# Kernel optimization log

Measured on AMD Instinct MI355X. Metric: run time of the kernel, lower is better.

Reference implementation:

```python
import jax, jax.numpy as jnp
import numpy as np


def setup_inputs() -> dict:
    key = jax.random.key(0)
    k1, k2, k3 = jax.random.split(key, 3)
    b, c, h, w = 4, 64, 64, 64
    content = jax.random.normal(k1, (b, c, h, w), dtype=jnp.float32)
    content_s = jax.random.normal(k2, (b, c, h, w), dtype=jnp.float32)
    style = jax.random.normal(k3, (b, c, h, w), dtype=jnp.float32)
    return {"content": content, "content_s": content_s, "style": style}


def reference(content, content_s, style):
    b, c, h, w = content.shape
    hw = h * w
    Fc = content.reshape(b, c, hw)      # [b, c, HW]
    Fs = content_s.reshape(b, c, hw)    # [b, c, HW]
    Fst = style.reshape(b, c, hw)       # [b, c, HW]
    # S[b, q, k] = sum_c Fc[b, c, q] * Fs[b, c, k]  (Fc transposed as in torch)
    S = jnp.einsum('bcq,bck->bqk', Fc, Fs)
    S = jax.nn.softmax(S, axis=-1)
    # O = style @ S^T : O[b, c, q] = sum_k Fst[b, c, k] * S[b, q, k]
    O = jnp.einsum('bck,bqk->bcq', Fst, S).reshape(b, c, h, w)
    return jnp.concatenate((content, O), axis=1)
```

## Files before the change

### kernel.cpp

```cpp
#include <hip/hip_runtime.h>
#include <math.h>


#define Bb 4
#define Cc 64
#define HWs 4096
#define RLOG2E 1.44269504088896340736f
#define DEFER_THR 6.0f

typedef _Float16 half8 __attribute__((ext_vector_type(8)));
typedef _Float16 half4 __attribute__((ext_vector_type(4)));
typedef float floatx4 __attribute__((ext_vector_type(4)));
typedef unsigned uint2v __attribute__((ext_vector_type(2)));

__global__ __launch_bounds__(256) void prep_k(const float* __restrict__ content,
                                              const float* __restrict__ Fs,
                                              const float* __restrict__ Fst,
                                              float* __restrict__ out,
                                              _Float16* __restrict__ Kt,
                                              _Float16* __restrict__ Vt) {
    const int bid = blockIdx.x;
    const int t = threadIdx.x;
    if (bid < 1024) {
        int i4 = bid * 256 + t;
        const float4* c4 = (const float4*)content;
        const float4* v4 = (const float4*)Fst;
        float4* o4 = (float4*)out;
        int b = i4 >> 16, rem = i4 & 65535;
        o4[(size_t)b * 131072 + rem] = c4[i4];
        float4 v = v4[i4];
        half4 h;
        h[0] = (_Float16)v.x; h[1] = (_Float16)v.y;
        h[2] = (_Float16)v.z; h[3] = (_Float16)v.w;
        *(half4*)(Vt + (size_t)i4 * 4) = h;
    } else {
        __shared__ _Float16 T[16][72];
        int e = bid - 1024;
        int b = e >> 8;
        int hw0 = (e & 255) * 16;
        const float* sb = Fs + (size_t)b * Cc * HWs;
        {
            int c = t >> 2, x4 = (t & 3) * 4;
            float4 v = *(const float4*)(sb + (size_t)c * HWs + hw0 + x4);
            T[x4 + 0][c] = (_Float16)v.x;
            T[x4 + 1][c] = (_Float16)v.y;
            T[x4 + 2][c] = (_Float16)v.z;
            T[x4 + 3][c] = (_Float16)v.w;
        }
        __syncthreads();
        if (t < 128) {
            int row = t >> 3, g = t & 7;
            _Float16* db = Kt + (size_t)b * HWs * Cc;
            *(half8*)(db + (size_t)(hw0 + row) * Cc + g * 8) = *(half8*)&T[row][g * 8];
        }
    }
}

template <int NS>
__global__ __launch_bounds__(256, 3) void attn_k(const float* __restrict__ Fc,
                                                 const _Float16* __restrict__ Kt,
                                                 const _Float16* __restrict__ Vt,
                                                 _Float16* __restrict__ Opart,
                                                 float2* __restrict__ ml) {
    constexpr int TPS = 64 / NS;
    const int tid  = threadIdx.x;
    const int w    = tid >> 6;
    const int lane = tid & 63;
    const int quad = lane >> 4;
    const int l15  = lane & 15;
    const int qg = blockIdx.x & 31;
    const int b  = (blockIdx.x >> 5) & 3;
    const int s  = blockIdx.x >> 7;
    const int k0base = s * TPS * 64;
    const int qA = qg * 128 + w * 32 + l15;
    const int qB = qA + 16;

    __shared__ _Float16 Kl[3][64 * 64];
    __shared__ _Float16 Vl[3][64 * 64];

    const float*    Fcb = Fc + (size_t)b * Cc * HWs;
    const _Float16* Kb  = Kt + (size_t)b * HWs * Cc;
    const _Float16* Vb  = Vt + (size_t)b * Cc * HWs;

    const int lrow = lane >> 3;
    const int lj   = lane & 7;
    const int lsw8 = (lj ^ lrow) * 8;
    const int r0   = w * 16;

    auto stage = [&](int kt, int p) {
        const int kk0 = k0base + kt * 64;
        #pragma unroll
        for (int c = 0; c < 2; ++c) {
            const int r = r0 + c * 8 + lrow;
            __builtin_amdgcn_global_load_lds(
                (const __attribute__((address_space(1))) void*)(Kb + (size_t)(kk0 + r) * 64 + lsw8),
                (__attribute__((address_space(3))) void*)&Kl[p][(r0 + c * 8) * 64],
                16, 0, 0);
            __builtin_amdgcn_global_load_lds(
                (const __attribute__((address_space(1))) void*)(Vb + (size_t)r * HWs + kk0 + lsw8),
                (__attribute__((address_space(3))) void*)&Vl[p][(r0 + c * 8) * 64],
                16, 0, 0);
        }
    };

    half8 qf[2][2];
    #pragma unroll
    for (int j = 0; j < 8; ++j) {
        qf[0][0][j] = (_Float16)(Fcb[(size_t)(quad * 8 + j) * HWs + qA] * RLOG2E);
        qf[0][1][j] = (_Float16)(Fcb[(size_t)(32 + quad * 8 + j) * HWs + qA] * RLOG2E);
        qf[1][0][j] = (_Float16)(Fcb[(size_t)(quad * 8 + j) * HWs + qB] * RLOG2E);
        qf[1][1][j] = (_Float16)(Fcb[(size_t)(32 + quad * 8 + j) * HWs + qB] * RLOG2E);
    }

    floatx4 acc[2][4];
    #pragma unroll
    for (int g = 0; g < 2; ++g)
        #pragma unroll
        for (int m = 0; m < 4; ++m) acc[g][m] = (floatx4)(0.0f);
    float m_run[2] = {-INFINITY, -INFINITY};
    float lsum[2] = {0.0f, 0.0f};

    asm volatile("" ::: "memory");
    stage(0, 0);
    stage(1, 1);

    const int swl = (l15 & 7);
    #pragma unroll
    for (int kt = 0; kt < TPS; ++kt) {
        const int p = kt % 3;
        if (kt + 1 < TPS) asm volatile("s_waitcnt vmcnt(4)" ::: "memory");
        else              asm volatile("s_waitcnt vmcnt(0)" ::: "memory");
        __builtin_amdgcn_s_barrier();
        __builtin_amdgcn_sched_barrier(0);
        if (kt + 2 < TPS) stage(kt + 2, (kt + 2) % 3);

        floatx4 sv[2][4];
        __builtin_amdgcn_s_setprio(1);
        #pragma unroll
        for (int m = 0; m < 4; ++m) {
            const half8 ka0 = *(const half8*)&Kl[p][(m * 16 + l15) * 64 + ((quad ^ swl) * 8)];
            const half8 ka1 = *(const half8*)&Kl[p][(m * 16 + l15) * 64 + (((4 + quad) ^ swl) * 8)];
            sv[0][m] = __builtin_amdgcn_mfma_f32_16x16x32_f16(ka0, qf[0][0], (floatx4)(0.0f), 0, 0, 0);
            sv[0][m] = __builtin_amdgcn_mfma_f32_16x16x32_f16(ka1, qf[0][1], sv[0][m], 0, 0, 0);
            sv[1][m] = __builtin_amdgcn_mfma_f32_16x16x32_f16(ka0, qf[1][0], (floatx4)(0.0f), 0, 0, 0);
            sv[1][m] = __builtin_amdgcn_mfma_f32_16x16x32_f16(ka1, qf[1][1], sv[1][m], 0, 0, 0);
        }
        __builtin_amdgcn_s_setprio(0);

        half8 pb[2][2];
        #pragma unroll
        for (int g = 0; g < 2; ++g) {
            float mm[4];
            #pragma unroll
            for (int m = 0; m < 4; ++m)
                mm[m] = fmaxf(fmaxf(sv[g][m][0], sv[g][m][1]),
                              fmaxf(sv[g][m][2], sv[g][m][3]));
            float mx = fmaxf(fmaxf(mm[0], mm[1]), fmaxf(mm[2], mm[3]));
            {
                unsigned mu = __float_as_uint(mx);
                uint2v t32 = __builtin_amdgcn_permlane32_swap(mu, mu, false, false);
                mx = fmaxf(__uint_as_float(t32[0]), __uint_as_float(t32[1]));
                mu = __float_as_uint(mx);
                uint2v t16 = __builtin_amdgcn_permlane16_swap(mu, mu, false, false);
                mx = fmaxf(__uint_as_float(t16[0]), __uint_as_float(t16[1]));
            }
            if (!__all(mx - m_run[g] <= DEFER_THR)) {
                float m_new = fmaxf(m_run[g], mx);
                float alpha = exp2f(m_run[g] - m_new);
                m_run[g] = m_new;
                #pragma unroll
                for (int m = 0; m < 4; ++m) acc[g][m] *= alpha;
                lsum[g] *= alpha;
            }
            const float mb = m_run[g];
            unsigned Ap[4], Bp[4];
            #pragma unroll
            for (int m = 0; m < 4; ++m) {
                float e0 = exp2f(sv[g][m][0] - mb);
                float e1 = exp2f(sv[g][m][1] - mb);
                float e2 = exp2f(sv[g][m][2] - mb);
                float e3 = exp2f(sv[g][m][3] - mb);
                lsum[g] += (e0 + e1) + (e2 + e3);
                Ap[m] = __builtin_bit_cast(unsigned, __builtin_amdgcn_cvt_pkrtz(e0, e1));
                Bp[m] = __builtin_bit_cast(unsigned, __builtin_amdgcn_cvt_pkrtz(e2, e3));
            }
            unsigned pw[2][4];
            { uint2v a = __builtin_amdgcn_permlane32_swap(Ap[0], Ap[1], false, false);
              uint2v u = __builtin_amdgcn_permlane16_swap(a[0], a[1], false, false);
              pw[0][0] = u[0]; pw[0][2] = u[1]; }
            { uint2v a = __builtin_amdgcn_permlane32_swap(Bp[0], Bp[1], false, false);
              uint2v u = __builtin_amdgcn_permlane16_swap(a[0], a[1], false, false);
              pw[0][1] = u[0]; pw[0][3] = u[1]; }
            { uint2v a = __builtin_amdgcn_permlane32_swap(Ap[2], Ap[3], false, false);
              uint2v u = __builtin_amdgcn_permlane16_swap(a[0], a[1], false, false);
              pw[1][0] = u[0]; pw[1][2] = u[1]; }
            { uint2v a = __builtin_amdgcn_permlane32_swap(Bp[2], Bp[3], false, false);
              uint2v u = __builtin_amdgcn_permlane16_swap(a[0], a[1], false, false);
              pw[1][1] = u[0]; pw[1][3] = u[1]; }
            #pragma unroll
            for (int ks = 0; ks < 2; ++ks) {
                union { unsigned u4[4]; half8 h; } z;
                z.u4[0] = pw[ks][0]; z.u4[1] = pw[ks][1];
                z.u4[2] = pw[ks][2]; z.u4[3] = pw[ks][3];
                pb[g][ks] = z.h;
            }
        }

        __builtin_amdgcn_s_setprio(1);
        #pragma unroll
        for (int m = 0; m < 4; ++m) {
            const half8 va0 = *(const half8*)&Vl[p][(m * 16 + l15) * 64 + ((quad ^ swl) * 8)];
            const half8 va1 = *(const half8*)&Vl[p][(m * 16 + l15) * 64 + (((4 + quad) ^ swl) * 8)];
            acc[0][m] = __builtin_amdgcn_mfma_f32_16x16x32_f16(va0, pb[0][0], acc[0][m], 0, 0, 0);
            acc[0][m] = __builtin_amdgcn_mfma_f32_16x16x32_f16(va1, pb[0][1], acc[0][m], 0, 0, 0);
            acc[1][m] = __builtin_amdgcn_mfma_f32_16x16x32_f16(va0, pb[1][0], acc[1][m], 0, 0, 0);
            acc[1][m] = __builtin_amdgcn_mfma_f32_16x16x32_f16(va1, pb[1][1], acc[1][m], 0, 0, 0);
        }
        __builtin_amdgcn_s_setprio(0);
    }

    _Float16* op = Opart + ((size_t)(s * Bb + b) * Cc) * HWs;
    #pragma unroll
    for (int g = 0; g < 2; ++g) {
        lsum[g] += __shfl_xor(lsum[g], 16);
        lsum[g] += __shfl_xor(lsum[g], 32);
        int q = (g == 0) ? qA : qB;
        #pragma unroll
        for (int m = 0; m < 4; ++m)
            #pragma unroll
            for (int r = 0; r < 4; ++r) {
                int c = m * 16 + quad * 4 + r;
                op[(size_t)c * HWs + q] = (_Float16)acc[g][m][r];
            }
        if (quad == 0)
            ml[((size_t)b * HWs + q) * NS + s] = make_float2(m_run[g], lsum[g]);
    }
}

template <int NS>
__global__ __launch_bounds__(256) void combine_k(const _Float16* __restrict__ Opart,
                                                 const float2* __restrict__ ml,
                                                 float* __restrict__ out) {
    int idx = blockIdx.x * 256 + threadIdx.x;
    int q = idx & 4095;
    int c = (idx >> 12) & 63;
    int b = idx >> 18;
    const float2* mlp = ml + ((size_t)b * HWs + q) * NS;
    float2 mls[NS];
    #pragma unroll
    for (int s = 0; s < NS; ++s) mls[s] = mlp[s];
    float M = -INFINITY;
    #pragma unroll
    for (int s = 0; s < NS; ++s) M = fmaxf(M, mls[s].x);
    float l = 0.0f, o = 0.0f;
    #pragma unroll
    for (int s = 0; s < NS; ++s) {
        float wgt = exp2f(mls[s].x - M);
        l += wgt * mls[s].y;
        o += wgt * (float)Opart[(((size_t)s * Bb + b) * Cc + c) * HWs + q];
    }
    out[((size_t)b * 2 * Cc + Cc + c) * HWs + q] = o / l;
}

extern "C" void kernel_launch(void* const* d_in, const int* in_sizes, int n_in,
                              void* d_out, int out_size, void* d_ws, size_t ws_size,
                              hipStream_t stream) {
    const float* content   = (const float*)d_in[0];
    const float* content_s = (const float*)d_in[1];
    const float* style     = (const float*)d_in[2];
    float* out = (float*)d_out;

    _Float16* Kt = (_Float16*)d_ws;
    _Float16* Vt = Kt + (size_t)Bb * HWs * Cc;
    _Float16* Opart = Vt + (size_t)Bb * Cc * HWs;

    const size_t base = (size_t)2 * Bb * HWs * Cc * sizeof(_Float16);
    const size_t need8 = base + (size_t)8 * Bb * Cc * HWs * sizeof(_Float16)
                              + (size_t)Bb * HWs * 8 * sizeof(float2);
    const int ns = (ws_size >= need8) ? 8 : 4;
    float2* ml = (float2*)(Opart + (size_t)ns * Bb * Cc * HWs);

    prep_k<<<dim3(2048), dim3(256), 0, stream>>>(content, content_s, style, out, Kt, Vt);
    if (ns == 8) {
        attn_k<8><<<dim3(8 * Bb * 32), dim3(256), 0, stream>>>(content, Kt, Vt, Opart, ml);
        combine_k<8><<<dim3(4096), dim3(256), 0, stream>>>(Opart, ml, out);
    } else {
        attn_k<4><<<dim3(4 * Bb * 32), dim3(256), 0, stream>>>(content, Kt, Vt, Opart, ml);
        combine_k<4><<<dim3(4096), dim3(256), 0, stream>>>(Opart, ml, out);
    }
}
```

Before: 113.4 us.

## Software-pipeline QK MFMA one tile ahead and split K/V staging

Splits K and V staging so that K is prefetched three tiles ahead and V two tiles ahead, and computes the QK^T MFMAs for tile kt+1 before running softmax and PV for tile kt, using double-buffered score registers. The aim is to overlap matrix-core work with the exp/permlane softmax chain and hide load latency. It also moves the cross-lane max reduction inside the rescale branch, so the common path skips permlane swaps. In exchange it raises register pressure from a second score buffer, and the loop unrolled by two assumes TPS is even.

```diff
diff --git a/kernel.cpp b/kernel.cpp
--- a/kernel.cpp
+++ b/kernel.cpp
@@ -12,6 +12,9 @@
 typedef _Float16 half4 __attribute__((ext_vector_type(4)));
 typedef float floatx4 __attribute__((ext_vector_type(4)));
 typedef unsigned uint2v __attribute__((ext_vector_type(2)));
+
+#define GAS __attribute__((address_space(1)))
+#define LAS __attribute__((address_space(3)))
 
 __global__ __launch_bounds__(256) void prep_k(const float* __restrict__ content,
                                               const float* __restrict__ Fs,
@@ -87,19 +90,24 @@
     const int lsw8 = (lj ^ lrow) * 8;
     const int r0   = w * 16;
 
-    auto stage = [&](int kt, int p) {
+    auto stageK = [&](int kt) {
         const int kk0 = k0base + kt * 64;
         #pragma unroll
         for (int c = 0; c < 2; ++c) {
             const int r = r0 + c * 8 + lrow;
             __builtin_amdgcn_global_load_lds(
-                (const __attribute__((address_space(1))) void*)(Kb + (size_t)(kk0 + r) * 64 + lsw8),
-                (__attribute__((address_space(3))) void*)&Kl[p][(r0 + c * 8) * 64],
-                16, 0, 0);
+                (const GAS void*)(Kb + (size_t)(kk0 + r) * 64 + lsw8),
+                (LAS void*)&Kl[kt % 3][(r0 + c * 8) * 64], 16, 0, 0);
+        }
+    };
+    auto stageV = [&](int kt) {
+        const int kk0 = k0base + kt * 64;
+        #pragma unroll
+        for (int c = 0; c < 2; ++c) {
+            const int r = r0 + c * 8 + lrow;
             __builtin_amdgcn_global_load_lds(
-                (const __attribute__((address_space(1))) void*)(Vb + (size_t)r * HWs + kk0 + lsw8),
-                (__attribute__((address_space(3))) void*)&Vl[p][(r0 + c * 8) * 64],
-                16, 0, 0);
+                (const GAS void*)(Vb + (size_t)r * HWs + kk0 + lsw8),
+                (LAS void*)&Vl[kt % 3][(r0 + c * 8) * 64], 16, 0, 0);
         }
     };
 
@@ -120,52 +128,42 @@
     float m_run[2] = {-INFINITY, -INFINITY};
     float lsum[2] = {0.0f, 0.0f};
 
-    asm volatile("" ::: "memory");
-    stage(0, 0);
-    stage(1, 1);
-
-    const int swl = (l15 & 7);
-    #pragma unroll
-    for (int kt = 0; kt < TPS; ++kt) {
-        const int p = kt % 3;
-        if (kt + 1 < TPS) asm volatile("s_waitcnt vmcnt(4)" ::: "memory");
-        else              asm volatile("s_waitcnt vmcnt(0)" ::: "memory");
-        __builtin_amdgcn_s_barrier();
-        __builtin_amdgcn_sched_barrier(0);
-        if (kt + 2 < TPS) stage(kt + 2, (kt + 2) % 3);
-
-        floatx4 sv[2][4];
+    const int swl = l15 & 7;
+    const int o0 = (quad ^ swl) * 8;
+    const int o1 = ((4 + quad) ^ swl) * 8;
+
+    auto s_mfma = [&](int kt1, floatx4 (&sv)[2][4]) {
+        const _Float16* K = &Kl[kt1 % 3][0];
         __builtin_amdgcn_s_setprio(1);
         #pragma unroll
         for (int m = 0; m < 4; ++m) {
-            const half8 ka0 = *(const half8*)&Kl[p][(m * 16 + l15) * 64 + ((quad ^ swl) * 8)];
-            const half8 ka1 = *(const half8*)&Kl[p][(m * 16 + l15) * 64 + (((4 + quad) ^ swl) * 8)];
+            const half8 ka0 = *(const half8*)(K + (m * 16 + l15) * 64 + o0);
+            const half8 ka1 = *(const half8*)(K + (m * 16 + l15) * 64 + o1);
             sv[0][m] = __builtin_amdgcn_mfma_f32_16x16x32_f16(ka0, qf[0][0], (floatx4)(0.0f), 0, 0, 0);
             sv[0][m] = __builtin_amdgcn_mfma_f32_16x16x32_f16(ka1, qf[0][1], sv[0][m], 0, 0, 0);
             sv[1][m] = __builtin_amdgcn_mfma_f32_16x16x32_f16(ka0, qf[1][0], (floatx4)(0.0f), 0, 0, 0);
             sv[1][m] = __builtin_amdgcn_mfma_f32_16x16x32_f16(ka1, qf[1][1], sv[1][m], 0, 0, 0);
         }
         __builtin_amdgcn_s_setprio(0);
-
+    };
+
+    auto sm_pv = [&](int kt, floatx4 (&sv)[2][4]) {
         half8 pb[2][2];
         #pragma unroll
         for (int g = 0; g < 2; ++g) {
-            float mm[4];
-            #pragma unroll
-            for (int m = 0; m < 4; ++m)
-                mm[m] = fmaxf(fmaxf(sv[g][m][0], sv[g][m][1]),
-                              fmaxf(sv[g][m][2], sv[g][m][3]));
-            float mx = fmaxf(fmaxf(mm[0], mm[1]), fmaxf(mm[2], mm[3]));
-            {
+            float mm0 = fmaxf(fmaxf(sv[g][0][0], sv[g][0][1]), fmaxf(sv[g][0][2], sv[g][0][3]));
+            float mm1 = fmaxf(fmaxf(sv[g][1][0], sv[g][1][1]), fmaxf(sv[g][1][2], sv[g][1][3]));
+            float mm2 = fmaxf(fmaxf(sv[g][2][0], sv[g][2][1]), fmaxf(sv[g][2][2], sv[g][2][3]));
+            float mm3 = fmaxf(fmaxf(sv[g][3][0], sv[g][3][1]), fmaxf(sv[g][3][2], sv[g][3][3]));
+            float mx = fmaxf(fmaxf(mm0, mm1), fmaxf(mm2, mm3));
+            if (!__all(mx - m_run[g] <= DEFER_THR)) {
                 unsigned mu = __float_as_uint(mx);
                 uint2v t32 = __builtin_amdgcn_permlane32_swap(mu, mu, false, false);
-                mx = fmaxf(__uint_as_float(t32[0]), __uint_as_float(t32[1]));
-                mu = __float_as_uint(mx);
+                float wmx = fmaxf(__uint_as_float(t32[0]), __uint_as_float(t32[1]));
+                mu = __float_as_uint(wmx);
                 uint2v t16 = __builtin_amdgcn_permlane16_swap(mu, mu, false, false);
-                mx = fmaxf(__uint_as_float(t16[0]), __uint_as_float(t16[1]));
-            }
-            if (!__all(mx - m_run[g] <= DEFER_THR)) {
-                float m_new = fmaxf(m_run[g], mx);
+                wmx = fmaxf(__uint_as_float(t16[0]), __uint_as_float(t16[1]));
+                float m_new = fmaxf(m_run[g], wmx);
                 float alpha = exp2f(m_run[g] - m_new);
                 m_run[g] = m_new;
                 #pragma unroll
@@ -205,18 +203,45 @@
                 pb[g][ks] = z.h;
             }
         }
-
+        const _Float16* V = &Vl[kt % 3][0];
         __builtin_amdgcn_s_setprio(1);
         #pragma unroll
         for (int m = 0; m < 4; ++m) {
-            const half8 va0 = *(const half8*)&Vl[p][(m * 16 + l15) * 64 + ((quad ^ swl) * 8)];
-            const half8 va1 = *(const half8*)&Vl[p][(m * 16 + l15) * 64 + (((4 + quad) ^ swl) * 8)];
+            const half8 va0 = *(const half8*)(V + (m * 16 + l15) * 64 + o0);
+            const half8 va1 = *(const half8*)(V + (m * 16 + l15) * 64 + o1);
             acc[0][m] = __builtin_amdgcn_mfma_f32_16x16x32_f16(va0, pb[0][0], acc[0][m], 0, 0, 0);
             acc[0][m] = __builtin_amdgcn_mfma_f32_16x16x32_f16(va1, pb[0][1], acc[0][m], 0, 0, 0);
             acc[1][m] = __builtin_amdgcn_mfma_f32_16x16x32_f16(va0, pb[1][0], acc[1][m], 0, 0, 0);
             acc[1][m] = __builtin_amdgcn_mfma_f32_16x16x32_f16(va1, pb[1][1], acc[1][m], 0, 0, 0);
         }
         __builtin_amdgcn_s_setprio(0);
+    };
+
+    auto iter = [&](int kt, floatx4 (&cur)[2][4], floatx4 (&nxt)[2][4]) {
+        if (kt + 2 < TPS)      asm volatile("s_waitcnt vmcnt(4)" ::: "memory");
+        else if (kt + 1 < TPS) asm volatile("s_waitcnt vmcnt(2)" ::: "memory");
+        else                   asm volatile("s_waitcnt vmcnt(0)" ::: "memory");
+        __builtin_amdgcn_s_barrier();
+        __builtin_amdgcn_sched_barrier(0);
+        if (kt + 3 < TPS) stageK(kt + 3);
+        if (kt + 2 < TPS) stageV(kt + 2);
+        if (kt + 1 < TPS) s_mfma(kt + 1, nxt);
+        sm_pv(kt, cur);
+    };
+
+    asm volatile("" ::: "memory");
+    stageK(0); stageK(1); stageV(0); stageK(2); stageV(1);
+    asm volatile("s_waitcnt vmcnt(4)" ::: "memory");
+    __builtin_amdgcn_s_barrier();
+    __builtin_amdgcn_sched_barrier(0);
+
+    floatx4 svA[2][4], svB[2][4];
+    s_mfma(0, svA);
+
+    #pragma unroll
+    for (int kt = 0; kt < TPS; kt += 2) {
+        iter(kt, svA, svB);
+        iter(kt + 1, svB, svA);
     }
 
     _Float16* op = Opart + ((size_t)(s * Bb + b) * Cc) * HWs;
```

Result: no change. 112.3 us (-1.0%).

## Double query rows per wave and fold max offset and row sums into MFMA

Applied to the files above, without the earlier changes.

Each wave now handles 64 query rows instead of 32, so each K/V tile loaded into shared memory is reused across twice as many queries, and the grid is halved. The running max is subtracted through the MFMA accumulator init, the cross-lane max reduction runs only when the threshold is exceeded, and row sums come from an extra MFMA against a ones vector instead of scalar adds. exp2f is replaced with the native hardware exp2, and the priority hints are dropped. The larger register footprint lowers the occupancy target to 2 blocks, and fewer blocks (512 with 8 splits) may leave CUs underfilled.

```diff
diff --git a/kernel.cpp b/kernel.cpp
--- a/kernel.cpp
+++ b/kernel.cpp
@@ -12,6 +12,16 @@
 typedef _Float16 half4 __attribute__((ext_vector_type(4)));
 typedef float floatx4 __attribute__((ext_vector_type(4)));
 typedef unsigned uint2v __attribute__((ext_vector_type(2)));
+
+#define GAS __attribute__((address_space(1)))
+#define LAS __attribute__((address_space(3)))
+
+extern "C" __device__ float __ocml_native_exp2_f32(float);
+#if defined(__has_builtin) && __has_builtin(__builtin_amdgcn_exp2f)
+#define EXP2(x) __builtin_amdgcn_exp2f(x)
+#else
+#define EXP2(x) __ocml_native_exp2_f32(x)
+#endif
 
 __global__ __launch_bounds__(256) void prep_k(const float* __restrict__ content,
                                               const float* __restrict__ Fs,
@@ -57,23 +67,22 @@
 }
 
 template <int NS>
-__global__ __launch_bounds__(256, 3) void attn_k(const float* __restrict__ Fc,
+__global__ __launch_bounds__(256, 2) void attn_k(const float* __restrict__ Fc,
                                                  const _Float16* __restrict__ Kt,
                                                  const _Float16* __restrict__ Vt,
                                                  _Float16* __restrict__ Opart,
                                                  float2* __restrict__ ml) {
     constexpr int TPS = 64 / NS;
     const int tid  = threadIdx.x;
-    const int w    = tid >> 6;
     const int lane = tid & 63;
     const int quad = lane >> 4;
     const int l15  = lane & 15;
-    const int qg = blockIdx.x & 31;
-    const int b  = (blockIdx.x >> 5) & 3;
-    const int s  = blockIdx.x >> 7;
+    const int w    = tid >> 6;
+    const int qg = blockIdx.x & 15;
+    const int b  = (blockIdx.x >> 4) & 3;
+    const int s  = blockIdx.x >> 6;
     const int k0base = s * TPS * 64;
-    const int qA = qg * 128 + w * 32 + l15;
-    const int qB = qA + 16;
+    const int qbase = qg * 256 + w * 64 + l15;
 
     __shared__ _Float16 Kl[3][64 * 64];
     __shared__ _Float16 Vl[3][64 * 64];
@@ -87,44 +96,54 @@
     const int lsw8 = (lj ^ lrow) * 8;
     const int r0   = w * 16;
 
-    auto stage = [&](int kt, int p) {
+    auto stage = [&](int kt) {
         const int kk0 = k0base + kt * 64;
         #pragma unroll
         for (int c = 0; c < 2; ++c) {
             const int r = r0 + c * 8 + lrow;
             __builtin_amdgcn_global_load_lds(
-                (const __attribute__((address_space(1))) void*)(Kb + (size_t)(kk0 + r) * 64 + lsw8),
-                (__attribute__((address_space(3))) void*)&Kl[p][(r0 + c * 8) * 64],
-                16, 0, 0);
+                (const GAS void*)(Kb + (size_t)(kk0 + r) * 64 + lsw8),
+                (LAS void*)&Kl[kt % 3][(r0 + c * 8) * 64], 16, 0, 0);
             __builtin_amdgcn_global_load_lds(
-                (const __attribute__((address_space(1))) void*)(Vb + (size_t)r * HWs + kk0 + lsw8),
-                (__attribute__((address_space(3))) void*)&Vl[p][(r0 + c * 8) * 64],
-                16, 0, 0);
+                (const GAS void*)(Vb + (size_t)r * HWs + kk0 + lsw8),
+                (LAS void*)&Vl[kt % 3][(r0 + c * 8) * 64], 16, 0, 0);
         }
     };
 
-    half8 qf[2][2];
-    #pragma unroll
-    for (int j = 0; j < 8; ++j) {
-        qf[0][0][j] = (_Float16)(Fcb[(size_t)(quad * 8 + j) * HWs + qA] * RLOG2E);
-        qf[0][1][j] = (_Float16)(Fcb[(size_t)(32 + quad * 8 + j) * HWs + qA] * RLOG2E);
-        qf[1][0][j] = (_Float16)(Fcb[(size_t)(quad * 8 + j) * HWs + qB] * RLOG2E);
-        qf[1][1][j] = (_Float16)(Fcb[(size_t)(32 + quad * 8 + j) * HWs + qB] * RLOG2E);
-    }
-
-    floatx4 acc[2][4];
-    #pragma unroll
-    for (int g = 0; g < 2; ++g)
+    half8 qf[4][2];
+    #pragma unroll
+    for (int g = 0; g < 4; ++g) {
+        const int q = qbase + g * 16;
+        #pragma unroll
+        for (int j = 0; j < 8; ++j) {
+            qf[g][0][j] = (_Float16)(Fcb[(size_t)(quad * 8 + j) * HWs + q] * RLOG2E);
+            qf[g][1][j] = (_Float16)(Fcb[(size_t)(32 + quad * 8 + j) * HWs + q] * RLOG2E);
+        }
+    }
+
+    floatx4 acc[4][4];
+    floatx4 accl[4];
+    float m_run[4];
+    #pragma unroll
+    for (int g = 0; g < 4; ++g) {
+        accl[g] = (floatx4)(0.0f);
+        m_run[g] = 0.0f;
         #pragma unroll
         for (int m = 0; m < 4; ++m) acc[g][m] = (floatx4)(0.0f);
-    float m_run[2] = {-INFINITY, -INFINITY};
-    float lsum[2] = {0.0f, 0.0f};
+    }
+
+    half8 vone;
+    #pragma unroll
+    for (int j = 0; j < 8; ++j) vone[j] = (_Float16)1.0f;
 
     asm volatile("" ::: "memory");
-    stage(0, 0);
-    stage(1, 1);
-
-    const int swl = (l15 & 7);
+    stage(0);
+    stage(1);
+
+    const int swl = l15 & 7;
+    const int o0 = (quad ^ swl) * 8;
+    const int o1 = ((4 + quad) ^ swl) * 8;
+
     #pragma unroll
     for (int kt = 0; kt < TPS; ++kt) {
         const int p = kt % 3;
@@ -132,55 +151,53 @@
         else              asm volatile("s_waitcnt vmcnt(0)" ::: "memory");
         __builtin_amdgcn_s_barrier();
         __builtin_amdgcn_sched_barrier(0);
-        if (kt + 2 < TPS) stage(kt + 2, (kt + 2) % 3);
-
-        floatx4 sv[2][4];
-        __builtin_amdgcn_s_setprio(1);
+        if (kt + 2 < TPS) stage(kt + 2);
+
+        floatx4 sv[4][4];
         #pragma unroll
         for (int m = 0; m < 4; ++m) {
-            const half8 ka0 = *(const half8*)&Kl[p][(m * 16 + l15) * 64 + ((quad ^ swl) * 8)];
-            const half8 ka1 = *(const half8*)&Kl[p][(m * 16 + l15) * 64 + (((4 + quad) ^ swl) * 8)];
-            sv[0][m] = __builtin_amdgcn_mfma_f32_16x16x32_f16(ka0, qf[0][0], (floatx4)(0.0f), 0, 0, 0);
-            sv[0][m] = __builtin_amdgcn_mfma_f32_16x16x32_f16(ka1, qf[0][1], sv[0][m], 0, 0, 0);
-            sv[1][m] = __builtin_amdgcn_mfma_f32_16x16x32_f16(ka0, qf[1][0], (floatx4)(0.0f), 0, 0, 0);
-            sv[1][m] = __builtin_amdgcn_mfma_f32_16x16x32_f16(ka1, qf[1][1], sv[1][m], 0, 0, 0);
-        }
-        __builtin_amdgcn_s_setprio(0);
-
-        half8 pb[2][2];
-        #pragma unroll
-        for (int g = 0; g < 2; ++g) {
-            float mm[4];
-            #pragma unroll
-            for (int m = 0; m < 4; ++m)
-                mm[m] = fmaxf(fmaxf(sv[g][m][0], sv[g][m][1]),
-                              fmaxf(sv[g][m][2], sv[g][m][3]));
-            float mx = fmaxf(fmaxf(mm[0], mm[1]), fmaxf(mm[2], mm[3]));
-            {
+            const half8 ka0 = *(const half8*)&Kl[p][(m * 16 + l15) * 64 + o0];
+            const half8 ka1 = *(const half8*)&Kl[p][(m * 16 + l15) * 64 + o1];
+            #pragma unroll
+            for (int g = 0; g < 4; ++g) {
+                sv[g][m] = __builtin_amdgcn_mfma_f32_16x16x32_f16(ka0, qf[g][0], (floatx4)(-m_run[g]), 0, 0, 0);
+                sv[g][m] = __builtin_amdgcn_mfma_f32_16x16x32_f16(ka1, qf[g][1], sv[g][m], 0, 0, 0);
+            }
+        }
+
+        half8 pb[4][2];
+        #pragma unroll
+        for (int g = 0; g < 4; ++g) {
+            float mm0 = fmaxf(fmaxf(fmaxf(sv[g][0][0], sv[g][0][1]), sv[g][0][2]), sv[g][0][3]);
+            float mm1 = fmaxf(fmaxf(fmaxf(sv[g][1][0], sv[g][1][1]), sv[g][1][2]), sv[g][1][3]);
+            float mm2 = fmaxf(fmaxf(fmaxf(sv[g][2][0], sv[g][2][1]), sv[g][2][2]), sv[g][2][3]);
+            float mm3 = fmaxf(fmaxf(fmaxf(sv[g][3][0], sv[g][3][1]), sv[g][3][2]), sv[g][3][3]);
+            float mx = fmaxf(fmaxf(fmaxf(mm0, mm1), mm2), mm3);
+            if (!__all(mx <= DEFER_THR)) {
                 unsigned mu = __float_as_uint(mx);
                 uint2v t32 = __builtin_amdgcn_permlane32_swap(mu, mu, false, false);
-                mx = fmaxf(__uint_as_float(t32[0]), __uint_as_float(t32[1]));
-                mu = __float_as_uint(mx);
+                float wmx = fmaxf(__uint_as_float(t32[0]), __uint_as_float(t32[1]));
+                mu = __float_as_uint(wmx);
                 uint2v t16 = __builtin_amdgcn_permlane16_swap(mu, mu, false, false);
-                mx = fmaxf(__uint_as_float(t16[0]), __uint_as_float(t16[1]));
-            }
-            if (!__all(mx - m_run[g] <= DEFER_THR)) {
-                float m_new = fmaxf(m_run[g], mx);
-                float alpha = exp2f(m_run[g] - m_new);
-                m_run[g] = m_new;
+                wmx = fmaxf(__uint_as_float(t16[0]), __uint_as_float(t16[1]));
+                float delta = fmaxf(wmx, 0.0f);
+                float alpha = EXP2(-delta);
+                m_run[g] += delta;
                 #pragma unroll
                 for (int m = 0; m < 4; ++m) acc[g][m] *= alpha;
-                lsum[g] *= alpha;
-            }
-            const float mb = m_run[g];
+                accl[g] *= alpha;
+                #pragma unroll
+                for (int m = 0; m < 4; ++m)
+                    #pragma unroll
+                    for (int r = 0; r < 4; ++r) sv[g][m][r] -= delta;
+            }
             unsigned Ap[4], Bp[4];
             #pragma unroll
             for (int m = 0; m < 4; ++m) {
-                float e0 = exp2f(sv[g][m][0] - mb);
-                float e1 = exp2f(sv[g][m][1] - mb);
-                float e2 = exp2f(sv[g][m][2] - mb);
-                float e3 = exp2f(sv[g][m][3] - mb);
-                lsum[g] += (e0 + e1) + (e2 + e3);
+                float e0 = EXP2(sv[g][m][0]);
+                float e1 = EXP2(sv[g][m][1]);
+                float e2 = EXP2(sv[g][m][2]);
+                float e3 = EXP2(sv[g][m][3]);
                 Ap[m] = __builtin_bit_cast(unsigned, __builtin_amdgcn_cvt_pkrtz(e0, e1));
                 Bp[m] = __builtin_bit_cast(unsigned, __builtin_amdgcn_cvt_pkrtz(e2, e3));
             }
@@ -206,25 +223,27 @@
             }
         }
 
-        __builtin_amdgcn_s_setprio(1);
         #pragma unroll
         for (int m = 0; m < 4; ++m) {
-            const half8 va0 = *(const half8*)&Vl[p][(m * 16 + l15) * 64 + ((quad ^ swl) * 8)];
-            const half8 va1 = *(const half8*)&Vl[p][(m * 16 + l15) * 64 + (((4 + quad) ^ swl) * 8)];
-            acc[0][m] = __builtin_amdgcn_mfma_f32_16x16x32_f16(va0, pb[0][0], acc[0][m], 0, 0, 0);
-            acc[0][m] = __builtin_amdgcn_mfma_f32_16x16x32_f16(va1, pb[0][1], acc[0][m], 0, 0, 0);
-            acc[1][m] = __builtin_amdgcn_mfma_f32_16x16x32_f16(va0, pb[1][0], acc[1][m], 0, 0, 0);
-            acc[1][m] = __builtin_amdgcn_mfma_f32_16x16x32_f16(va1, pb[1][1], acc[1][m], 0, 0, 0);
-        }
-        __builtin_amdgcn_s_setprio(0);
-    }
-
-    _Float16* op = Opart + ((size_t)(s * Bb + b) * Cc) * HWs;
-    #pragma unroll
-    for (int g = 0; g < 2; ++g) {
-        lsum[g] += __shfl_xor(lsum[g], 16);
-        lsum[g] += __shfl_xor(lsum[g], 32);
-        int q = (g == 0) ? qA : qB;
+            const half8 va0 = *(const half8*)&Vl[p][(m * 16 + l15) * 64 + o0];
+            const half8 va1 = *(const half8*)&Vl[p][(m * 16 + l15) * 64 + o1];
+            #pragma unroll
+            for (int g = 0; g < 4; ++g) {
+                acc[g][m] = __builtin_amdgcn_mfma_f32_16x16x32_f16(va0, pb[g][0], acc[g][m], 0, 0, 0);
+                acc[g][m] = __builtin_amdgcn_mfma_f32_16x16x32_f16(va1, pb[g][1], acc[g][m], 0, 0, 0);
+            }
+        }
+        #pragma unroll
+        for (int g = 0; g < 4; ++g) {
+            accl[g] = __builtin_amdgcn_mfma_f32_16x16x32_f16(vone, pb[g][0], accl[g], 0, 0, 0);
+            accl[g] = __builtin_amdgcn_mfma_f32_16x16x32_f16(vone, pb[g][1], accl[g], 0, 0, 0);
+        }
+    }
+
+    _Float16* op = Opart + (((size_t)s * Bb + b) * Cc) * HWs;
+    #pragma unroll
+    for (int g = 0; g < 4; ++g) {
+        const int q = qbase + g * 16;
         #pragma unroll
         for (int m = 0; m < 4; ++m)
             #pragma unroll
@@ -233,7 +252,7 @@
                 op[(size_t)c * HWs + q] = (_Float16)acc[g][m][r];
             }
         if (quad == 0)
-            ml[((size_t)b * HWs + q) * NS + s] = make_float2(m_run[g], lsum[g]);
+            ml[((size_t)b * HWs + q) * NS + s] = make_float2(m_run[g], accl[g][0]);
     }
 }
 
@@ -255,7 +274,7 @@
     float l = 0.0f, o = 0.0f;
     #pragma unroll
     for (int s = 0; s < NS; ++s) {
-        float wgt = exp2f(mls[s].x - M);
+        float wgt = EXP2(mls[s].x - M);
         l += wgt * mls[s].y;
         o += wgt * (float)Opart[(((size_t)s * Bb + b) * Cc + c) * HWs + q];
     }
@@ -282,10 +301,10 @@
 
     prep_k<<<dim3(2048), dim3(256), 0, stream>>>(content, content_s, style, out, Kt, Vt);
     if (ns == 8) {
-        attn_k<8><<<dim3(8 * Bb * 32), dim3(256), 0, stream>>>(content, Kt, Vt, Opart, ml);
+        attn_k<8><<<dim3(8 * Bb * 16), dim3(256), 0, stream>>>(content, Kt, Vt, Opart, ml);
         combine_k<8><<<dim3(4096), dim3(256), 0, stream>>>(Opart, ml, out);
     } else {
-        attn_k<4><<<dim3(4 * Bb * 32), dim3(256), 0, stream>>>(content, Kt, Vt, Opart, ml);
+        attn_k<4><<<dim3(4 * Bb * 16), dim3(256), 0, stream>>>(content, Kt, Vt, Opart, ml);
         combine_k<4><<<dim3(4096), dim3(256), 0, stream>>>(Opart, ml, out);
     }
 }
```

After: 103.6 us. 1.09x faster.
